# Optimization experiments

Measured on AMD Instinct MI355X. Metric: run time of the kernel, lower is better.

The kernel has to match this reference:

```python
import jax, jax.numpy as jnp
import numpy as np

B, SQ, SK, D, DV = 8, 2048, 4096, 512, 256

def setup_inputs() -> dict:
    key = jax.random.key(0)
    k1, k2, k3, k4, k5 = jax.random.split(key, 5)
    X = jax.random.normal(k1, (B, SQ, D), dtype=jnp.float32)
    Y = jax.random.normal(k2, (SK, D), dtype=jnp.float32)
    Z = jax.random.normal(k3, (SK, D), dtype=jnp.float32)
    # Linear weights (torch stores [out, in]); scaled like default init
    W_k = jax.random.normal(k4, (D, D), dtype=jnp.float32) / np.sqrt(D)
    W_v = jax.random.normal(k5, (DV, D), dtype=jnp.float32) / np.sqrt(D)
    return {"X": X, "Y": Y, "Z": Z, "W_k": W_k, "W_v": W_v, "rate": 0}


def reference(X, Y, Z, W_k, W_v, rate):
    # key = W_k(Y).unsqueeze(0): [1, SK, D]; value = W_v(Z).unsqueeze(0): [1, SK, DV]
    key = (Y @ W_k.T)[None]
    value = (Z @ W_v.T)[None]
    # scores = X @ key^T / sqrt(d): [B, SQ, SK] (key batch dim broadcasts)
    scale = 1.0 / jnp.sqrt(jnp.asarray(X.shape[-1], dtype=X.dtype))
    scores = jnp.matmul(X, jnp.swapaxes(key, 1, 2)) * scale
    attn = jax.nn.softmax(scores, axis=-1)
    # dropout layers act as identity in eval mode
    out = jnp.matmul(attn, value)  # [B, SQ, DV]
    return out
```

## Files before the change

kernel.cpp:

```cpp
#include <hip/hip_runtime.h>
#include <hip/hip_bf16.h>

#define NB    8
#define SQN   2048
#define SKN   4096
#define DDIM  512
#define DVDIM 256
#define NROWS (NB*SQN)
#define NS    2
#define NJ    ((SKN/64)/NS)

typedef __attribute__((ext_vector_type(8)))  short bf16x8;
typedef __attribute__((ext_vector_type(4)))  short bf16x4;
typedef __attribute__((ext_vector_type(4)))  float f32x4;
typedef __attribute__((ext_vector_type(16))) float f32x16;

__device__ __forceinline__ short f2bf(float f) {
    unsigned u = __float_as_uint(f);
    return (short)((u + 0x7FFFu + ((u >> 16) & 1u)) >> 16);
}

#define BAR_LGKM() do {                                                       \
    asm volatile("s_waitcnt lgkmcnt(0)" ::: "memory");                        \
    __builtin_amdgcn_sched_barrier(0);                                        \
    __builtin_amdgcn_s_barrier();                                             \
    __builtin_amdgcn_sched_barrier(0);                                        \
} while (0)

__global__ __launch_bounds__(256, 2) void proj_gemms(
    const float* __restrict__ Y, const float* __restrict__ Z,
    const float* __restrict__ Wk, const float* __restrict__ Wv,
    unsigned short* __restrict__ keyb, unsigned short* __restrict__ vtb)
{
    __shared__ short sA[64*128];
    __shared__ short sB[64*128];
    const float *A, *Bm;
    unsigned short* C;
    int m0, n0;
    const bool kpath = (blockIdx.z == 0);
    if (kpath) {
        A = Y; Bm = Wk; C = keyb;
        m0 = blockIdx.x * 64; n0 = blockIdx.y * 64;
    } else {
        int lin = blockIdx.x * 8 + blockIdx.y;
        if (lin >= 256) return;
        A = Wv; Bm = Z; C = vtb;
        m0 = (lin >> 6) * 64; n0 = (lin & 63) * 64;
    }
    const int tid  = threadIdx.x;
    const int wave = tid >> 6;
    const int lane = tid & 63;
    const int quad = lane >> 4;
    const int l15  = lane & 15;

    f32x4 acc[4];
    #pragma unroll
    for (int n = 0; n < 4; ++n) { acc[n][0]=0.f; acc[n][1]=0.f; acc[n][2]=0.f; acc[n][3]=0.f; }

    float4 ra[8], rb[8];
    #pragma unroll
    for (int it = 0; it < 8; ++it) {
        int f = it*1024 + tid*4, row = f >> 7, col = f & 127;
        ra[it] = *(const float4*)(A  + (size_t)(m0+row)*DDIM + col);
        rb[it] = *(const float4*)(Bm + (size_t)(n0+row)*DDIM + col);
    }

    for (int kc = 0; kc < DDIM; kc += 128) {
        __syncthreads();
        #pragma unroll
        for (int it = 0; it < 8; ++it) {
            int f = it*1024 + tid*4;
            bf16x4 a4; a4[0]=f2bf(ra[it].x); a4[1]=f2bf(ra[it].y); a4[2]=f2bf(ra[it].z); a4[3]=f2bf(ra[it].w);
            *(bf16x4*)(sA + f) = a4;
            bf16x4 b4; b4[0]=f2bf(rb[it].x); b4[1]=f2bf(rb[it].y); b4[2]=f2bf(rb[it].z); b4[3]=f2bf(rb[it].w);
            *(bf16x4*)(sB + f) = b4;
        }
        __syncthreads();
        if (kc + 128 < DDIM) {
            #pragma unroll
            for (int it = 0; it < 8; ++it) {
                int f = it*1024 + tid*4, row = f >> 7, col = f & 127;
                ra[it] = *(const float4*)(A  + (size_t)(m0+row)*DDIM + kc + 128 + col);
                rb[it] = *(const float4*)(Bm + (size_t)(n0+row)*DDIM + kc + 128 + col);
            }
        }
        #pragma unroll
        for (int t = 0; t < 4; ++t) {
            bf16x8 af = *(const bf16x8*)(sA + (wave*16 + l15)*128 + t*32 + quad*8);
            #pragma unroll
            for (int n = 0; n < 4; ++n) {
                bf16x8 bfr = *(const bf16x8*)(sB + (n*16 + l15)*128 + t*32 + quad*8);
                acc[n] = __builtin_amdgcn_mfma_f32_16x16x32_bf16(af, bfr, acc[n], 0, 0, 0);
            }
        }
    }
    #pragma unroll
    for (int n = 0; n < 4; ++n)
        #pragma unroll
        for (int r = 0; r < 4; ++r) {
            int m  = m0 + wave*16 + quad*4 + r;
            int nn = n0 + n*16 + l15;
            unsigned short v = (unsigned short)f2bf(acc[n][r]);
            size_t off;
            if (kpath) {
                int J = m >> 6, kh = (m >> 5) & 1, ls = m & 31;
                int c = nn >> 7, tp = (nn >> 4) & 7, hd = (nn >> 3) & 1, d7 = nn & 7;
                off = (size_t)(((J*4 + c)*8 + tp)*2 + kh)*512 + (hd*32 + ls)*8 + d7;
            } else {
                int J = nn >> 6, g = (nn >> 4) & 3, hk = (nn >> 3) & 1, k7 = nn & 7;
                int wv = m >> 7, n2 = (m >> 5) & 3, lv = m & 31;
                off = (size_t)((J*8 + wv*4 + n2)*4 + g)*512 + (hk*32 + lv)*8 + k7;
            }
            C[off] = v;
        }
}

__global__ __launch_bounds__(128, 1) void attn_fused(
    const float* __restrict__ X,
    const unsigned short* __restrict__ Kb,
    const unsigned short* __restrict__ Vt,
    float* __restrict__ Opart,
    float* __restrict__ Mpart,
    float* __restrict__ Lpart)
{
    __shared__ __align__(16) char smem[74752];
    char* sQ   = smem;
    char* sPex = smem + 65536;
    float* sSt = (float*)(smem + 73728);

    const int tid  = threadIdx.x;
    const int wk   = tid >> 6;
    const int lane = tid & 63;
    const int l31  = lane & 31;
    const int hi   = lane >> 5;

    const int bid   = blockIdx.x;
    const int xcd   = bid & 7;
    const int slot  = bid >> 3;
    const int split = xcd >> 2;
    const int q0    = ((xcd & 3)*64 + slot) * 64;
    const float scale = 0.04419417382415922f * 1.4426950408889634f;

    {
        const float* xrow = X + (size_t)(q0 + wk*32 + l31)*DDIM + hi*8;
        char* qst = sQ + wk*32768;
        #pragma unroll
        for (int t2 = 0; t2 < 32; ++t2) {
            float4 a = *(const float4*)(xrow + t2*16);
            float4 b = *(const float4*)(xrow + t2*16 + 4);
            bf16x8 q;
            q[0]=f2bf(a.x*scale); q[1]=f2bf(a.y*scale); q[2]=f2bf(a.z*scale); q[3]=f2bf(a.w*scale);
            q[4]=f2bf(b.x*scale); q[5]=f2bf(b.y*scale); q[6]=f2bf(b.z*scale); q[7]=f2bf(b.w*scale);
            *(bf16x8*)(qst + t2*1024 + lane*16) = q;
        }
    }

    f32x16 o[2][4];
    #pragma unroll
    for (int g2 = 0; g2 < 2; ++g2)
        #pragma unroll
        for (int n = 0; n < 4; ++n)
            #pragma unroll
            for (int r = 0; r < 16; ++r) o[g2][n][r] = 0.f;
    float m_r[2] = {-1e30f, -1e30f};
    float l_r[2] = {0.f, 0.f};

    const int Jg0 = split * NJ;
    const char* kp = (const char*)Kb + (size_t)Jg0*65536 + wk*1024 + lane*16;
    const char* vp = (const char*)Vt + (size_t)Jg0*32768 + wk*16384 + lane*16;
    #define KOFF(h_, t_) ((size_t)((h_)>>1)*16384 + (size_t)((((h_)&1)*4 + (t_))*2)*1024)

    bf16x8 kf[3][4];
    bf16x8 vf[4][4];
    f32x16 sA_[2], sB_[2];

    BAR_LGKM();

    #define LD_KF(buf_, h_)                                                   \
        do { _Pragma("unroll")                                                \
             for (int t_ = 0; t_ < 4; ++t_)                                   \
                 kf[buf_][t_] = *(const bf16x8*)(kp + KOFF(h_, t_));          \
        } while (0)

    #define LD_V(half_, voff_)                                                \
        do { _Pragma("unroll")                                                \
             for (int gg_ = 0; gg_ < 2; ++gg_)                                \
                 _Pragma("unroll")                                            \
                 for (int n_ = 0; n_ < 4; ++n_)                               \
                     vf[(half_)*2 + gg_][n_] = *(const bf16x8*)(vp + (voff_)  \
                         + n_*4096 + ((half_)*2 + gg_)*1024);                 \
        } while (0)

    const char* qb = sQ + lane*16;

    #define QK_PH(SN_, buf_, h_)                                              \
        do {                                                                  \
            __builtin_amdgcn_s_setprio(1);                                    \
            _Pragma("unroll")                                                 \
            for (int t_ = 0; t_ < 4; ++t_) {                                  \
                bf16x8 q0_ = *(const bf16x8*)(qb + ((h_)*4 + t_)*1024);       \
                bf16x8 q1_ = *(const bf16x8*)(qb + 32768 + ((h_)*4 + t_)*1024);\
                SN_[0] = __builtin_amdgcn_mfma_f32_32x32x16_bf16(             \
                            kf[buf_][t_], q0_, SN_[0], 0, 0, 0);              \
                SN_[1] = __builtin_amdgcn_mfma_f32_32x32x16_bf16(             \
                            kf[buf_][t_], q1_, SN_[1], 0, 0, 0);              \
            }                                                                 \
            __builtin_amdgcn_s_setprio(0);                                    \
        } while (0)

    LD_KF(0, 0); LD_KF(1, 1);
    #pragma unroll
    for (int g2 = 0; g2 < 2; ++g2)
        #pragma unroll
        for (int r = 0; r < 16; ++r) sA_[g2][r] = 0.f;
    LD_KF(2, 2); QK_PH(sA_, 0, 0);
    LD_KF(0, 3); QK_PH(sA_, 1, 1);
    LD_KF(1, 4); QK_PH(sA_, 2, 2);
    LD_KF(2, 5); QK_PH(sA_, 0, 3);
    LD_KF(0, 6); QK_PH(sA_, 1, 4);
    LD_KF(1, 7); QK_PH(sA_, 2, 5);
    LD_V(0, 0);  QK_PH(sA_, 0, 6);
    LD_V(1, 0);  QK_PH(sA_, 1, 7);
    kp += 65536;
    LD_KF(0, 0); LD_KF(1, 1);

    #define ITER(jv, SC, SN)                                                  \
    {                                                                         \
        const bool hasN = (jv) + 1 < NJ;                                      \
                                   \
        float tmx[2];                                                         \
        _Pragma("unroll")                                                     \
        for (int g2 = 0; g2 < 2; ++g2) {                                      \
            float v = fmaxf(fmaxf(fmaxf(SC[g2][0],SC[g2][1]),fmaxf(SC[g2][2],SC[g2][3])), \
                            fmaxf(fmaxf(SC[g2][4],SC[g2][5]),fmaxf(SC[g2][6],SC[g2][7]))); \
            v = fmaxf(v, fmaxf(fmaxf(fmaxf(SC[g2][8],SC[g2][9]),fmaxf(SC[g2][10],SC[g2][11])), \
                               fmaxf(fmaxf(SC[g2][12],SC[g2][13]),fmaxf(SC[g2][14],SC[g2][15])))); \
            v = fmaxf(v, __shfl_xor(v, 32));                                  \
            tmx[g2] = v;                                                      \
            if (lane < 32) sSt[((wk*2 + g2)*2 + 0)*32 + lane] = v;            \
        }                                                                     \
                        \
        if (hasN) {                                                           \
            _Pragma("unroll")                                                 \
            for (int g2 = 0; g2 < 2; ++g2)                                    \
                _Pragma("unroll")                                             \
                for (int r = 0; r < 16; ++r) SN[g2][r] = 0.f;                 \
            LD_KF(2, 2); QK_PH(SN, 0, 0);                                     \
            LD_KF(0, 3); QK_PH(SN, 1, 1);                                     \
            LD_KF(1, 4); QK_PH(SN, 2, 2);                                     \
            LD_KF(2, 5); QK_PH(SN, 0, 3);                                     \
        }                                                                     \
        BAR_LGKM();                                           \
                                 \
        bool upd[2]; float mn[2], tsum[2], alpha[2];                          \
        bf16x8 pf[2][2];                                                      \
        _Pragma("unroll")                                                     \
        for (int g2 = 0; g2 < 2; ++g2) {                                      \
            float to = sSt[(((wk^1)*2 + g2)*2 + 0)*32 + l31];                 \
            float tj = fmaxf(tmx[g2], to);                                    \
            upd[g2] = tj > m_r[g2] + 8.0f;                 \
            mn[g2]  = upd[g2] ? tj : m_r[g2];                                 \
            alpha[g2] = upd[g2] ? exp2f(m_r[g2] - mn[g2]) : 1.0f;             \
            float ts = 0.f;                                                   \
            _Pragma("unroll")                                                 \
            for (int r = 0; r < 16; ++r) {                                    \
                float pv = exp2f(SC[g2][r] - mn[g2]); SC[g2][r] = pv; ts += pv; \
            }                                                                 \
            ts += __shfl_xor(ts, 32);                                         \
            tsum[g2] = ts;                                                    \
            if (lane < 32) sSt[((wk*2 + g2)*2 + 1)*32 + lane] = ts;           \
            _Pragma("unroll")                                                 \
            for (int ks = 0; ks < 2; ++ks) {                                  \
                int wA, wB, wC, wD;                                           \
                asm("v_cvt_pk_bf16_f32 %0, %1, %2" : "=v"(wA) : "v"(SC[g2][8*ks+0]), "v"(SC[g2][8*ks+1])); \
                asm("v_cvt_pk_bf16_f32 %0, %1, %2" : "=v"(wB) : "v"(SC[g2][8*ks+2]), "v"(SC[g2][8*ks+3])); \
                asm("v_cvt_pk_bf16_f32 %0, %1, %2" : "=v"(wC) : "v"(SC[g2][8*ks+4]), "v"(SC[g2][8*ks+5])); \
                asm("v_cvt_pk_bf16_f32 %0, %1, %2" : "=v"(wD) : "v"(SC[g2][8*ks+6]), "v"(SC[g2][8*ks+7])); \
                asm("v_permlane32_swap_b32 %0, %1" : "+v"(wA), "+v"(wC));     \
                asm("v_permlane32_swap_b32 %0, %1" : "+v"(wB), "+v"(wD));     \
                union { int w[4]; bf16x8 v; } u;                              \
                u.w[0] = wA; u.w[1] = wB; u.w[2] = wC; u.w[3] = wD;           \
                pf[g2][ks] = u.v;                                             \
                *(bf16x8*)(sPex + (g2*4 + wk*2 + ks)*1024 + lane*16) = u.v;   \
            }                                                                 \
        }                                                                     \
                               \
        if (hasN) {                                                           \
            LD_KF(0, 6); QK_PH(SN, 1, 4);                                     \
            LD_KF(1, 7); QK_PH(SN, 2, 5);                                     \
        }                                                                     \
        BAR_LGKM();                                           \
                      \
        _Pragma("unroll")                                                     \
        for (int g2 = 0; g2 < 2; ++g2) {                                      \
            float tso = sSt[(((wk^1)*2 + g2)*2 + 1)*32 + l31];                \
            l_r[g2] = l_r[g2]*alpha[g2] + (tsum[g2] + tso);                   \
            m_r[g2] = mn[g2];                                                 \
            if (__any(upd[g2])) {                                             \
                _Pragma("unroll")                                             \
                for (int r = 0; r < 16; ++r) {                                \
                    int row = (r&3) + 8*(r>>2) + 4*hi;                        \
                    float ar = __shfl(alpha[g2], row);                        \
                    _Pragma("unroll")                                         \
                    for (int n = 0; n < 4; ++n) o[g2][n][r] *= ar;            \
                }                                                             \
            }                                                                 \
        }                                                                     \
         \
        {                                                                     \
            const char* pb_ = sPex + lane*16;                                 \
            __builtin_amdgcn_s_setprio(1);                                    \
            _Pragma("unroll")                                                 \
            for (int g = 0; g < 4; ++g) {                                     \
                bf16x8 pa0 = ((g >> 1) == wk) ? pf[0][g & 1]                  \
                            : *(const bf16x8*)(pb_ + (0*4 + g)*1024);         \
                bf16x8 pa1 = ((g >> 1) == wk) ? pf[1][g & 1]                  \
                            : *(const bf16x8*)(pb_ + (1*4 + g)*1024);         \
                _Pragma("unroll")                                             \
                for (int n = 0; n < 4; ++n) {                                 \
                    o[0][n] = __builtin_amdgcn_mfma_f32_32x32x16_bf16(        \
                            pa0, vf[g][n], o[0][n], 0, 0, 0);                 \
                    o[1][n] = __builtin_amdgcn_mfma_f32_32x32x16_bf16(        \
                            pa1, vf[g][n], o[1][n], 0, 0, 0);                 \
                }                                                             \
            }                                                                 \
            __builtin_amdgcn_s_setprio(0);                                    \
        }                                                                     \
                \
        if (hasN) {                                                           \
            LD_V(0, 32768); QK_PH(SN, 0, 6);                                  \
            LD_V(1, 32768); QK_PH(SN, 1, 7);                                  \
            kp += 65536;                                                      \
            if ((jv) + 2 < NJ) { LD_KF(0, 0); LD_KF(1, 1); }                  \
        }                                                                     \
        vp += 32768;                                                          \
    }

    for (int j = 0; j < NJ; j += 2) {
        ITER(j,     sA_, sB_);
        ITER(j + 1, sB_, sA_);
    }
    #undef ITER
    #undef QK_PH
    #undef LD_V
    #undef LD_KF
    #undef KOFF

    const size_t base = (size_t)split * NROWS;
    #pragma unroll
    for (int g2 = 0; g2 < 2; ++g2) {
        const int gr0 = q0 + g2*32;
        if (wk == 0 && lane < 32) {
            Mpart[base + gr0 + lane] = m_r[g2];
            Lpart[base + gr0 + lane] = l_r[g2];
        }
        #pragma unroll
        for (int r = 0; r < 16; ++r) {
            int row = (r&3) + 8*(r>>2) + 4*hi;
            float* orow = Opart + (base + gr0 + row) * (size_t)DVDIM + wk*128;
            #pragma unroll
            for (int n = 0; n < 4; ++n)
                orow[n*32 + l31] = o[g2][n][r];
        }
    }
}

__global__ void combine_splits(
    const float* __restrict__ Opart, const float* __restrict__ Mpart,
    const float* __restrict__ Lpart, float* __restrict__ out)
{
    const int row = blockIdx.x * 4 + (threadIdx.x >> 6);
    const int dv4 = (threadIdx.x & 63) * 4;
    float M = -1e30f;
    #pragma unroll
    for (int s = 0; s < NS; ++s) M = fmaxf(M, Mpart[(size_t)s*NROWS + row]);
    float denom = 0.f;
    float4 acc = make_float4(0.f, 0.f, 0.f, 0.f);
    #pragma unroll
    for (int s = 0; s < NS; ++s) {
        float w = exp2f(Mpart[(size_t)s*NROWS + row] - M);
        denom += Lpart[(size_t)s*NROWS + row] * w;
        float4 ov = *(const float4*)(Opart + ((size_t)s*NROWS + row)*DVDIM + dv4);
        acc.x += ov.x*w; acc.y += ov.y*w; acc.z += ov.z*w; acc.w += ov.w*w;
    }
    float inv = 1.0f / denom;
    *(float4*)(out + (size_t)row*DVDIM + dv4)
        = make_float4(acc.x*inv, acc.y*inv, acc.z*inv, acc.w*inv);
}

extern "C" void kernel_launch(void* const* d_in, const int* in_sizes, int n_in,
                              void* d_out, int out_size, void* d_ws, size_t ws_size,
                              hipStream_t stream) {
    const float* X  = (const float*)d_in[0];
    const float* Y  = (const float*)d_in[1];
    const float* Z  = (const float*)d_in[2];
    const float* Wk = (const float*)d_in[3];
    const float* Wv = (const float*)d_in[4];
    float* out = (float*)d_out;

    char* ws = (char*)d_ws;
    unsigned short* keyb = (unsigned short*)ws;
    unsigned short* vtb  = (unsigned short*)(ws + (4u<<20));
    float* Opart = (float*)(ws + (6u<<20));
    float* Mpart = (float*)(ws + (6u<<20) + (size_t)NS*NROWS*DVDIM*4);
    float* Lpart = Mpart + (size_t)NS*NROWS;

    proj_gemms<<<dim3(64, 8, 2), dim3(256), 0, stream>>>(Y, Z, Wk, Wv, keyb, vtb);
    attn_fused<<<dim3(512), dim3(128), 0, stream>>>(
        X, keyb, vtb, Opart, Mpart, Lpart);
    combine_splits<<<dim3(NROWS/4), dim3(256), 0, stream>>>(Opart, Mpart, Lpart, out);
}
```

Measured before the change: 275.9 us.

## Halve query tile to 32 rows per block, doubling grid and occupancy

Each attention block now handles 32 query rows instead of 64. This halves the O accumulators, score registers and LDS footprint, allows two blocks per CU, and doubles the grid to 1024 blocks. V fragment loads are merged into one load issued after the next tile's QK phases. The cost is that every K/V tile is fetched from L2 twice as many times, and each K fragment load now feeds only one MFMA instead of two.

```diff
diff --git a/kernel.cpp b/kernel.cpp
--- a/kernel.cpp
+++ b/kernel.cpp
@@ -115,7 +115,7 @@
         }
 }
 
-__global__ __launch_bounds__(128, 1) void attn_fused(
+__global__ __launch_bounds__(128, 2) void attn_fused(
     const float* __restrict__ X,
     const unsigned short* __restrict__ Kb,
     const unsigned short* __restrict__ Vt,
@@ -123,10 +123,10 @@
     float* __restrict__ Mpart,
     float* __restrict__ Lpart)
 {
-    __shared__ __align__(16) char smem[74752];
+    __shared__ __align__(16) char smem[37376];
     char* sQ   = smem;
-    char* sPex = smem + 65536;
-    float* sSt = (float*)(smem + 73728);
+    char* sPex = smem + 32768;
+    float* sSt = (float*)(smem + 36864);
 
     const int tid  = threadIdx.x;
     const int wk   = tid >> 6;
@@ -138,32 +138,29 @@
     const int xcd   = bid & 7;
     const int slot  = bid >> 3;
     const int split = xcd >> 2;
-    const int q0    = ((xcd & 3)*64 + slot) * 64;
+    const int q0    = ((xcd & 3)*128 + slot) * 32;
     const float scale = 0.04419417382415922f * 1.4426950408889634f;
 
     {
-        const float* xrow = X + (size_t)(q0 + wk*32 + l31)*DDIM + hi*8;
-        char* qst = sQ + wk*32768;
-        #pragma unroll
-        for (int t2 = 0; t2 < 32; ++t2) {
+        const float* xrow = X + (size_t)(q0 + l31)*DDIM + hi*8;
+        #pragma unroll
+        for (int i = 0; i < 16; ++i) {
+            const int t2 = wk*16 + i;
             float4 a = *(const float4*)(xrow + t2*16);
             float4 b = *(const float4*)(xrow + t2*16 + 4);
             bf16x8 q;
             q[0]=f2bf(a.x*scale); q[1]=f2bf(a.y*scale); q[2]=f2bf(a.z*scale); q[3]=f2bf(a.w*scale);
             q[4]=f2bf(b.x*scale); q[5]=f2bf(b.y*scale); q[6]=f2bf(b.z*scale); q[7]=f2bf(b.w*scale);
-            *(bf16x8*)(qst + t2*1024 + lane*16) = q;
-        }
-    }
-
-    f32x16 o[2][4];
-    #pragma unroll
-    for (int g2 = 0; g2 < 2; ++g2)
-        #pragma unroll
-        for (int n = 0; n < 4; ++n)
-            #pragma unroll
-            for (int r = 0; r < 16; ++r) o[g2][n][r] = 0.f;
-    float m_r[2] = {-1e30f, -1e30f};
-    float l_r[2] = {0.f, 0.f};
+            *(bf16x8*)(sQ + t2*1024 + lane*16) = q;
+        }
+    }
+
+    f32x16 o[4];
+    #pragma unroll
+    for (int n = 0; n < 4; ++n)
+        #pragma unroll
+        for (int r = 0; r < 16; ++r) o[n][r] = 0.f;
+    float m_r = -1e30f, l_r = 0.f;
 
     const int Jg0 = split * NJ;
     const char* kp = (const char*)Kb + (size_t)Jg0*65536 + wk*1024 + lane*16;
@@ -172,7 +169,7 @@
 
     bf16x8 kf[3][4];
     bf16x8 vf[4][4];
-    f32x16 sA_[2], sB_[2];
+    f32x16 sA_, sB_;
 
     BAR_LGKM();
 
@@ -182,69 +179,61 @@
                  kf[buf_][t_] = *(const bf16x8*)(kp + KOFF(h_, t_));          \
         } while (0)
 
-    #define LD_V(half_, voff_)                                                \
+    #define LD_V4(voff_)                                                      \
         do { _Pragma("unroll")                                                \
-             for (int gg_ = 0; gg_ < 2; ++gg_)                                \
+             for (int g_ = 0; g_ < 4; ++g_)                                   \
                  _Pragma("unroll")                                            \
                  for (int n_ = 0; n_ < 4; ++n_)                               \
-                     vf[(half_)*2 + gg_][n_] = *(const bf16x8*)(vp + (voff_)  \
-                         + n_*4096 + ((half_)*2 + gg_)*1024);                 \
+                     vf[g_][n_] = *(const bf16x8*)(vp + (voff_)               \
+                         + n_*4096 + g_*1024);                                \
         } while (0)
 
     const char* qb = sQ + lane*16;
 
-    #define QK_PH(SN_, buf_, h_)                                              \
+    #define QK_PH(S_, buf_, h_)                                               \
         do {                                                                  \
             __builtin_amdgcn_s_setprio(1);                                    \
             _Pragma("unroll")                                                 \
             for (int t_ = 0; t_ < 4; ++t_) {                                  \
-                bf16x8 q0_ = *(const bf16x8*)(qb + ((h_)*4 + t_)*1024);       \
-                bf16x8 q1_ = *(const bf16x8*)(qb + 32768 + ((h_)*4 + t_)*1024);\
-                SN_[0] = __builtin_amdgcn_mfma_f32_32x32x16_bf16(             \
-                            kf[buf_][t_], q0_, SN_[0], 0, 0, 0);              \
-                SN_[1] = __builtin_amdgcn_mfma_f32_32x32x16_bf16(             \
-                            kf[buf_][t_], q1_, SN_[1], 0, 0, 0);              \
+                bf16x8 qv_ = *(const bf16x8*)(qb + ((h_)*4 + t_)*1024);       \
+                S_ = __builtin_amdgcn_mfma_f32_32x32x16_bf16(                 \
+                        kf[buf_][t_], qv_, S_, 0, 0, 0);                      \
             }                                                                 \
             __builtin_amdgcn_s_setprio(0);                                    \
         } while (0)
 
     LD_KF(0, 0); LD_KF(1, 1);
     #pragma unroll
-    for (int g2 = 0; g2 < 2; ++g2)
-        #pragma unroll
-        for (int r = 0; r < 16; ++r) sA_[g2][r] = 0.f;
+    for (int r = 0; r < 16; ++r) sA_[r] = 0.f;
     LD_KF(2, 2); QK_PH(sA_, 0, 0);
     LD_KF(0, 3); QK_PH(sA_, 1, 1);
     LD_KF(1, 4); QK_PH(sA_, 2, 2);
     LD_KF(2, 5); QK_PH(sA_, 0, 3);
     LD_KF(0, 6); QK_PH(sA_, 1, 4);
     LD_KF(1, 7); QK_PH(sA_, 2, 5);
-    LD_V(0, 0);  QK_PH(sA_, 0, 6);
-    LD_V(1, 0);  QK_PH(sA_, 1, 7);
+    LD_V4(0);    QK_PH(sA_, 0, 6);
+    QK_PH(sA_, 1, 7);
     kp += 65536;
     LD_KF(0, 0); LD_KF(1, 1);
 
     #define ITER(jv, SC, SN)                                                  \
     {                                                                         \
         const bool hasN = (jv) + 1 < NJ;                                      \
-                                   \
-        float tmx[2];                                                         \
-        _Pragma("unroll")                                                     \
-        for (int g2 = 0; g2 < 2; ++g2) {                                      \
-            float v = fmaxf(fmaxf(fmaxf(SC[g2][0],SC[g2][1]),fmaxf(SC[g2][2],SC[g2][3])), \
-                            fmaxf(fmaxf(SC[g2][4],SC[g2][5]),fmaxf(SC[g2][6],SC[g2][7]))); \
-            v = fmaxf(v, fmaxf(fmaxf(fmaxf(SC[g2][8],SC[g2][9]),fmaxf(SC[g2][10],SC[g2][11])), \
-                               fmaxf(fmaxf(SC[g2][12],SC[g2][13]),fmaxf(SC[g2][14],SC[g2][15])))); \
+                                          \
+        float tmx;                                                            \
+        {                                                                     \
+            float v = fmaxf(fmaxf(fmaxf(SC[0],SC[1]),fmaxf(SC[2],SC[3])),     \
+                            fmaxf(fmaxf(SC[4],SC[5]),fmaxf(SC[6],SC[7])));    \
+            v = fmaxf(v, fmaxf(fmaxf(fmaxf(SC[8],SC[9]),fmaxf(SC[10],SC[11])), \
+                               fmaxf(fmaxf(SC[12],SC[13]),fmaxf(SC[14],SC[15])))); \
             v = fmaxf(v, __shfl_xor(v, 32));                                  \
-            tmx[g2] = v;                                                      \
-            if (lane < 32) sSt[((wk*2 + g2)*2 + 0)*32 + lane] = v;            \
+            tmx = v;                                                          \
+            if (lane < 32) sSt[(wk*2 + 0)*32 + lane] = v;                     \
         }                                                                     \
                         \
         if (hasN) {                                                           \
             _Pragma("unroll")                                                 \
-            for (int g2 = 0; g2 < 2; ++g2)                                    \
-                _Pragma("unroll")                                             \
-                for (int r = 0; r < 16; ++r) SN[g2][r] = 0.f;                 \
+            for (int r = 0; r < 16; ++r) SN[r] = 0.f;                         \
             LD_KF(2, 2); QK_PH(SN, 0, 0);                                     \
             LD_KF(0, 3); QK_PH(SN, 1, 1);                                     \
             LD_KF(1, 4); QK_PH(SN, 2, 2);                                     \
@@ -252,36 +241,35 @@
         }                                                                     \
         BAR_LGKM();                                           \
                                  \
-        bool upd[2]; float mn[2], tsum[2], alpha[2];                          \
-        bf16x8 pf[2][2];                                                      \
-        _Pragma("unroll")                                                     \
-        for (int g2 = 0; g2 < 2; ++g2) {                                      \
-            float to = sSt[(((wk^1)*2 + g2)*2 + 0)*32 + l31];                 \
-            float tj = fmaxf(tmx[g2], to);                                    \
-            upd[g2] = tj > m_r[g2] + 8.0f;                 \
-            mn[g2]  = upd[g2] ? tj : m_r[g2];                                 \
-            alpha[g2] = upd[g2] ? exp2f(m_r[g2] - mn[g2]) : 1.0f;             \
+        bool upd; float mn, tsum, alpha;                                      \
+        bf16x8 pf[2];                                                         \
+        {                                                                     \
+            float to = sSt[((wk^1)*2 + 0)*32 + l31];                          \
+            float tj = fmaxf(tmx, to);                                        \
+            upd = tj > m_r + 8.0f;                         \
+            mn  = upd ? tj : m_r;                                             \
+            alpha = upd ? exp2f(m_r - mn) : 1.0f;                             \
             float ts = 0.f;                                                   \
             _Pragma("unroll")                                                 \
             for (int r = 0; r < 16; ++r) {                                    \
-                float pv = exp2f(SC[g2][r] - mn[g2]); SC[g2][r] = pv; ts += pv; \
+                float pv = exp2f(SC[r] - mn); SC[r] = pv; ts += pv;           \
             }                                                                 \
             ts += __shfl_xor(ts, 32);                                         \
-            tsum[g2] = ts;                                                    \
-            if (lane < 32) sSt[((wk*2 + g2)*2 + 1)*32 + lane] = ts;           \
+            tsum = ts;                                                        \
+            if (lane < 32) sSt[(wk*2 + 1)*32 + lane] = ts;                    \
             _Pragma("unroll")                                                 \
             for (int ks = 0; ks < 2; ++ks) {                                  \
                 int wA, wB, wC, wD;                                           \
-                asm("v_cvt_pk_bf16_f32 %0, %1, %2" : "=v"(wA) : "v"(SC[g2][8*ks+0]), "v"(SC[g2][8*ks+1])); \
-                asm("v_cvt_pk_bf16_f32 %0, %1, %2" : "=v"(wB) : "v"(SC[g2][8*ks+2]), "v"(SC[g2][8*ks+3])); \
-                asm("v_cvt_pk_bf16_f32 %0, %1, %2" : "=v"(wC) : "v"(SC[g2][8*ks+4]), "v"(SC[g2][8*ks+5])); \
-                asm("v_cvt_pk_bf16_f32 %0, %1, %2" : "=v"(wD) : "v"(SC[g2][8*ks+6]), "v"(SC[g2][8*ks+7])); \
+                asm("v_cvt_pk_bf16_f32 %0, %1, %2" : "=v"(wA) : "v"(SC[8*ks+0]), "v"(SC[8*ks+1])); \
+                asm("v_cvt_pk_bf16_f32 %0, %1, %2" : "=v"(wB) : "v"(SC[8*ks+2]), "v"(SC[8*ks+3])); \
+                asm("v_cvt_pk_bf16_f32 %0, %1, %2" : "=v"(wC) : "v"(SC[8*ks+4]), "v"(SC[8*ks+5])); \
+                asm("v_cvt_pk_bf16_f32 %0, %1, %2" : "=v"(wD) : "v"(SC[8*ks+6]), "v"(SC[8*ks+7])); \
                 asm("v_permlane32_swap_b32 %0, %1" : "+v"(wA), "+v"(wC));     \
                 asm("v_permlane32_swap_b32 %0, %1" : "+v"(wB), "+v"(wD));     \
                 union { int w[4]; bf16x8 v; } u;                              \
                 u.w[0] = wA; u.w[1] = wB; u.w[2] = wC; u.w[3] = wD;           \
-                pf[g2][ks] = u.v;                                             \
-                *(bf16x8*)(sPex + (g2*4 + wk*2 + ks)*1024 + lane*16) = u.v;   \
+                pf[ks] = u.v;                                                 \
+                *(bf16x8*)(sPex + (wk*2 + ks)*1024 + lane*16) = u.v;          \
             }                                                                 \
         }                                                                     \
                                \
@@ -290,46 +278,41 @@
             LD_KF(1, 7); QK_PH(SN, 2, 5);                                     \
         }                                                                     \
         BAR_LGKM();                                           \
-                      \
-        _Pragma("unroll")                                                     \
-        for (int g2 = 0; g2 < 2; ++g2) {                                      \
-            float tso = sSt[(((wk^1)*2 + g2)*2 + 1)*32 + l31];                \
-            l_r[g2] = l_r[g2]*alpha[g2] + (tsum[g2] + tso);                   \
-            m_r[g2] = mn[g2];                                                 \
-            if (__any(upd[g2])) {                                             \
+                                               \
+        {                                                                     \
+            float tso = sSt[((wk^1)*2 + 1)*32 + l31];                         \
+            l_r = l_r*alpha + (tsum + tso);                                   \
+            m_r = mn;                                                         \
+            if (__any(upd)) {                                                 \
                 _Pragma("unroll")                                             \
                 for (int r = 0; r < 16; ++r) {                                \
                     int row = (r&3) + 8*(r>>2) + 4*hi;                        \
-                    float ar = __shfl(alpha[g2], row);                        \
+                    float ar = __shfl(alpha, row);                            \
                     _Pragma("unroll")                                         \
-                    for (int n = 0; n < 4; ++n) o[g2][n][r] *= ar;            \
+                    for (int n = 0; n < 4; ++n) o[n][r] *= ar;                \
                 }                                                             \
             }                                                                 \
         }                                                                     \
-         \
+                   \
         {                                                                     \
             const char* pb_ = sPex + lane*16;                                 \
             __builtin_amdgcn_s_setprio(1);                                    \
             _Pragma("unroll")                                                 \
             for (int g = 0; g < 4; ++g) {                                     \
-                bf16x8 pa0 = ((g >> 1) == wk) ? pf[0][g & 1]                  \
-                            : *(const bf16x8*)(pb_ + (0*4 + g)*1024);         \
-                bf16x8 pa1 = ((g >> 1) == wk) ? pf[1][g & 1]                  \
-                            : *(const bf16x8*)(pb_ + (1*4 + g)*1024);         \
+                bf16x8 pa = ((g >> 1) == wk) ? pf[g & 1]                      \
+                            : *(const bf16x8*)(pb_ + g*1024);                 \
                 _Pragma("unroll")                                             \
-                for (int n = 0; n < 4; ++n) {                                 \
-                    o[0][n] = __builtin_amdgcn_mfma_f32_32x32x16_bf16(        \
-                            pa0, vf[g][n], o[0][n], 0, 0, 0);                 \
-                    o[1][n] = __builtin_amdgcn_mfma_f32_32x32x16_bf16(        \
-                            pa1, vf[g][n], o[1][n], 0, 0, 0);                 \
-                }                                                             \
+                for (int n = 0; n < 4; ++n)                                   \
+                    o[n] = __builtin_amdgcn_mfma_f32_32x32x16_bf16(           \
+                            pa, vf[g][n], o[n], 0, 0, 0);                     \
             }                                                                 \
             __builtin_amdgcn_s_setprio(0);                                    \
         }                                                                     \
-                \
+             \
         if (hasN) {                                                           \
-            LD_V(0, 32768); QK_PH(SN, 0, 6);                                  \
-            LD_V(1, 32768); QK_PH(SN, 1, 7);                                  \
+            QK_PH(SN, 0, 6);                                                  \
+            QK_PH(SN, 1, 7);                                                  \
+            LD_V4(32768);                                                     \
             kp += 65536;                                                      \
             if ((jv) + 2 < NJ) { LD_KF(0, 0); LD_KF(1, 1); }                  \
         }                                                                     \
@@ -342,26 +325,22 @@
     }
     #undef ITER
     #undef QK_PH
-    #undef LD_V
+    #undef LD_V4
     #undef LD_KF
     #undef KOFF
 
     const size_t base = (size_t)split * NROWS;
-    #pragma unroll
-    for (int g2 = 0; g2 < 2; ++g2) {
-        const int gr0 = q0 + g2*32;
-        if (wk == 0 && lane < 32) {
-            Mpart[base + gr0 + lane] = m_r[g2];
-            Lpart[base + gr0 + lane] = l_r[g2];
-        }
-        #pragma unroll
-        for (int r = 0; r < 16; ++r) {
-            int row = (r&3) + 8*(r>>2) + 4*hi;
-            float* orow = Opart + (base + gr0 + row) * (size_t)DVDIM + wk*128;
-            #pragma unroll
-            for (int n = 0; n < 4; ++n)
-                orow[n*32 + l31] = o[g2][n][r];
-        }
+    if (wk == 0 && lane < 32) {
+        Mpart[base + q0 + lane] = m_r;
+        Lpart[base + q0 + lane] = l_r;
+    }
+    #pragma unroll
+    for (int r = 0; r < 16; ++r) {
+        int row = (r&3) + 8*(r>>2) + 4*hi;
+        float* orow = Opart + (base + q0 + row) * (size_t)DVDIM + wk*128;
+        #pragma unroll
+        for (int n = 0; n < 4; ++n)
+            orow[n*32 + l31] = o[n][r];
     }
 }
 
@@ -406,7 +385,7 @@
     float* Lpart = Mpart + (size_t)NS*NROWS;
 
     proj_gemms<<<dim3(64, 8, 2), dim3(256), 0, stream>>>(Y, Z, Wk, Wv, keyb, vtb);
-    attn_fused<<<dim3(512), dim3(128), 0, stream>>>(
+    attn_fused<<<dim3(1024), dim3(128), 0, stream>>>(
         X, keyb, vtb, Opart, Mpart, Lpart);
     combine_splits<<<dim3(NROWS/4), dim3(256), 0, stream>>>(Opart, Mpart, Lpart, out);
 }
```

Measured after the change: 259.1 us. -6.1%, faster.
